# Optimization experiments

Hardware: AMD Instinct MI355X
Metric: run time of the kernel (lower is better)

## Reference

```python
import jax, jax.numpy as jnp
import numpy as np

B, N, M, D = 32, 1024, 576, 768

def setup_inputs() -> dict:
    key = jax.random.key(0)
    k1, k2 = jax.random.split(key)
    hidden_states = jax.random.normal(k1, (B, N, D), dtype=jnp.float32)
    img_hidden_state = jax.random.normal(k2, (B, M, D), dtype=jnp.float32)
    return {"hidden_states": hidden_states, "img_hidden_state": img_hidden_state}

def reference(hidden_states, img_hidden_state):
    # Unscaled cross-attention: softmax(Q K^T) V with Q=text, K=V=image features.
    scores = jnp.einsum('bnd,bmd->bnm', hidden_states, img_hidden_state)  # [B,N,M]
    probs = jax.nn.softmax(scores, axis=-1)
    fusion_output = jnp.einsum('bnm,bmd->bnd', probs, img_hidden_state)   # [B,N,D]
    return fusion_output
```

## Files before the change

### kernel.cpp

```cpp
#include <hip/hip_runtime.h>

typedef float f32x4 __attribute__((ext_vector_type(4)));
typedef _Float16 h8 __attribute__((ext_vector_type(8)));
typedef unsigned short us8 __attribute__((ext_vector_type(8)));

#define DEV __device__ __forceinline__
#define SBARRIER() asm volatile("s_barrier" ::: "memory")
#define LGKM0()    asm volatile("s_waitcnt lgkmcnt(0)" ::: "memory")
#define VMCNT3()   asm volatile("s_waitcnt vmcnt(3)" ::: "memory")
#define VMCNT0()   asm volatile("s_waitcnt vmcnt(0)" ::: "memory")
#define SCHED0()   __builtin_amdgcn_sched_barrier(0)

constexpr int Bb = 32, Nn = 1024, Mm = 576, Dd = 768;
constexpr float L2E = 1.44269504088896340736f;

constexpr size_t KF_ELEMS = (size_t)Bb * 36 * 24 * 512;

DEV unsigned short f2h(float x) {
  _Float16 h = (_Float16)x;
  return __builtin_bit_cast(unsigned short, h);
}
DEV void gll16(const void* g, void* l) {
  __builtin_amdgcn_global_load_lds(
      (const __attribute__((address_space(1))) void*)g,
      (__attribute__((address_space(3))) void*)l, 16, 0, 0);
}

__global__ __launch_bounds__(256)
void fusion_prep(const float* __restrict__ K, unsigned short* __restrict__ Kf,
                 unsigned short* __restrict__ Vf)
{
  __shared__ float ks[64][33];
  const int t   = threadIdx.x;
  const int blk = blockIdx.x;
  const int b    = blk / 18;
  const int r2   = blk % 18;
  const int rt   = r2 >> 1;
  const int half = r2 & 1;
  const int l    = t & 63;

  const int row0 = t >> 3, c40 = t & 7;
  const int row1 = (t + 256) >> 3;
  const float* Kb = K + ((size_t)(b * Mm + rt * 64)) * Dd;

  const int kvt_l = t >> 6;
  const int kf_r  = kvt_l * 16 + (l & 15);
  const int kf_c  = (l >> 4) * 8;
  const int kc_l = t >> 7;
  const int dtl  = (t >> 6) & 1;
  const int vf_r = kc_l * 32 + (l >> 4) * 8;
  const int vf_c = dtl * 16 + (l & 15);

#pragma unroll 1
  for (int dc = half * 12; dc < half * 12 + 12; ++dc) {
    __syncthreads();
    f32x4 v0 = *(const f32x4*)(Kb + (size_t)row0 * Dd + dc * 32 + c40 * 4);
    f32x4 v1 = *(const f32x4*)(Kb + (size_t)row1 * Dd + dc * 32 + c40 * 4);
    *(f32x4*)&ks[row0][c40 * 4] = v0;
    *(f32x4*)&ks[row1][c40 * 4] = v1;
    __syncthreads();
    {
      us8 h;
#pragma unroll
      for (int j = 0; j < 8; ++j) h[j] = f2h(ks[kf_r][kf_c + j]);
      *(us8*)&Kf[(((size_t)((b * 36 + rt * 4 + kvt_l) * 24 + dc)) << 9) + l * 8] = h;
    }
    {
      us8 o;
#pragma unroll
      for (int j = 0; j < 8; ++j) o[j] = f2h(ks[vf_r + j][vf_c]);
      *(us8*)&Vf[(((size_t)((b * 18 + rt * 2 + kc_l) * 48 + dc * 2 + dtl)) << 9) + l * 8] = o;
    }
  }
}

__global__ __launch_bounds__(1024, 1)
void fusion_main(const float* __restrict__ Q, const unsigned short* __restrict__ Kf,
                 const unsigned short* __restrict__ Vf, float* __restrict__ Out)
{
  __shared__ alignas(16) unsigned char lds[147456];
  __shared__ float sRa[4][128];
  __shared__ float sRb[4][128];

  const int tid  = threadIdx.x;
  const int lane = tid & 63;
  const int w    = tid >> 6;
  const int g    = lane >> 4;
  const int ln   = lane & 15;
  const int wq   = w >> 2;
  const int wkv  = w & 3;
  const int wq2  = w >> 3;
  const int wd8  = w & 7;

  const bool loader  = (w < 12);
  const bool qstager = (w >= 12);

  const int bid = blockIdx.x;
  const int xcd = bid & 7, ii = bid >> 3;
  const int b  = (xcd << 2) | (ii >> 3);
  const int q0 = (ii & 7) * 128;

  const float* Qb = Q + ((size_t)(b * Nn + q0)) * Dd;
  const unsigned char* KfB = (const unsigned char*)Kf + ((size_t)(b * 36 * 24) << 10);
  const unsigned short* VfB = Vf + ((size_t)(b * 18 * 48) << 9);

  const int u0 = w * 3;
  const int t256 = tid & 255;
  const int s0 = t256, s1 = t256 + 256;
  const int qt0 = s0 >> 6, l0 = s0 & 63;
  const int qt1 = s1 >> 6, l1 = s1 & 63;
  const float* qsrc0 = Qb + (size_t)(qt0 * 16 + (l0 & 15)) * Dd + (l0 >> 4) * 8;
  const float* qsrc1 = Qb + (size_t)(qt1 * 16 + (l1 & 15)) * Dd + (l1 >> 4) * 8;
  unsigned char* qd0 = lds + 110592 + qt0 * 1024 + l0 * 16;
  unsigned char* qd1 = lds + 110592 + qt1 * 1024 + l1 * 16;

  {
    f32x4 a0, a1, b0, b1;
    if (qstager) {
      a0 = *(const f32x4*)qsrc0; a1 = *(const f32x4*)(qsrc0 + 4);
      b0 = *(const f32x4*)qsrc1; b1 = *(const f32x4*)(qsrc1 + 4);
    }
    SCHED0();
    if (loader) {
#pragma unroll
      for (int j = 0; j < 3; ++j)
        gll16(KfB + ((size_t)((u0 + j) * 24) << 10) + (lane << 4), lds + (u0 + j) * 1024);
#pragma unroll
      for (int j = 0; j < 3; ++j)
        gll16(KfB + ((size_t)((u0 + j) * 24 + 1) << 10) + (lane << 4), lds + 36864 + (u0 + j) * 1024);
    }
    if (qstager) {
      us8 h0, h1;
#pragma unroll
      for (int k = 0; k < 4; ++k) {
        h0[k]   = f2h(a0[k] * L2E);
        h0[k+4] = f2h(a1[k] * L2E);
        h1[k]   = f2h(b0[k] * L2E);
        h1[k+4] = f2h(b1[k] * L2E);
      }
      *(us8*)qd0 = h0;
      *(us8*)qd1 = h1;
    }
    if (loader) { VMCNT3(); }
    LGKM0();
    SBARRIER();
    SCHED0();
  }

  f32x4 acc[2][9];
#pragma unroll
  for (int mt = 0; mt < 2; ++mt)
#pragma unroll
    for (int nt = 0; nt < 9; ++nt) acc[mt][nt] = (f32x4){0.f, 0.f, 0.f, 0.f};

#pragma unroll 1
  for (int c = 0; c < 24; ++c) {
    f32x4 a0, a1, b0, b1;
    if (qstager && c < 23) {
      const size_t off = (size_t)(c + 1) * 32;
      a0 = *(const f32x4*)(qsrc0 + off); a1 = *(const f32x4*)(qsrc0 + off + 4);
      b0 = *(const f32x4*)(qsrc1 + off); b1 = *(const f32x4*)(qsrc1 + off + 4);
    }
    SCHED0();
    if (loader && c < 22) {
      unsigned char* dst = lds + ((c + 2) % 3) * 36864;
#pragma unroll
      for (int j = 0; j < 3; ++j) {
        const int u = u0 + j;
        gll16(KfB + ((size_t)(u * 24 + c + 2) << 10) + (lane << 4), dst + u * 1024);
      }
    }
    const unsigned char* qb = lds + 110592 + (c & 1) * 8192;
    const unsigned char* kb = lds + (c % 3) * 36864;
    h8 qh[2];
#pragma unroll
    for (int mt = 0; mt < 2; ++mt)
      qh[mt] = *(const h8*)(qb + (wq * 2 + mt) * 1024 + lane * 16);
    __builtin_amdgcn_s_setprio(1);
#pragma unroll
    for (int nt = 0; nt < 9; ++nt) {
      const h8 kf = *(const h8*)(kb + (wkv * 9 + nt) * 1024 + lane * 16);
#pragma unroll
      for (int mt = 0; mt < 2; ++mt)
        acc[mt][nt] = __builtin_amdgcn_mfma_f32_16x16x32_f16(qh[mt], kf, acc[mt][nt], 0, 0, 0);
    }
    __builtin_amdgcn_s_setprio(0);
    SCHED0();
    if (qstager && c < 23) {
      us8 h0, h1;
#pragma unroll
      for (int k = 0; k < 4; ++k) {
        h0[k]   = f2h(a0[k] * L2E);
        h0[k+4] = f2h(a1[k] * L2E);
        h1[k]   = f2h(b0[k] * L2E);
        h1[k+4] = f2h(b1[k] * L2E);
      }
      *(us8*)(qd0 + ((c + 1) & 1) * 8192) = h0;
      *(us8*)(qd1 + ((c + 1) & 1) * 8192) = h1;
    }
    if (loader) {
      if (c <= 21) { VMCNT3(); }
      else         { VMCNT0(); }
    }
    LGKM0();
    SBARRIER();
    SCHED0();
  }

  float pm[2][4];
#pragma unroll
  for (int mt = 0; mt < 2; ++mt)
#pragma unroll
    for (int i2 = 0; i2 < 4; ++i2) {
      float v = acc[mt][0][i2];
#pragma unroll
      for (int nt = 1; nt < 9; ++nt) v = fmaxf(v, acc[mt][nt][i2]);
      pm[mt][i2] = v;
    }
#pragma unroll
  for (int mk = 1; mk < 16; mk <<= 1)
#pragma unroll
    for (int mt = 0; mt < 2; ++mt)
#pragma unroll
      for (int i2 = 0; i2 < 4; ++i2)
        pm[mt][i2] = fmaxf(pm[mt][i2], __shfl_xor(pm[mt][i2], mk, 64));
  if (ln == 0) {
#pragma unroll
    for (int mt = 0; mt < 2; ++mt)
#pragma unroll
      for (int i2 = 0; i2 < 4; ++i2)
        sRa[wkv][wq * 32 + mt * 16 + g * 4 + i2] = pm[mt][i2];
  }
  __syncthreads();

  float mfin[2][4], ps[2][4];
#pragma unroll
  for (int mt = 0; mt < 2; ++mt)
#pragma unroll
    for (int i2 = 0; i2 < 4; ++i2) {
      const int rw = wq * 32 + mt * 16 + g * 4 + i2;
      mfin[mt][i2] = fmaxf(fmaxf(sRa[0][rw], sRa[1][rw]), fmaxf(sRa[2][rw], sRa[3][rw]));
      ps[mt][i2] = 0.f;
    }
#pragma unroll
  for (int mt = 0; mt < 2; ++mt)
#pragma unroll
    for (int nt = 0; nt < 9; ++nt)
#pragma unroll
      for (int i2 = 0; i2 < 4; ++i2) {
        const float p = exp2f(acc[mt][nt][i2] - mfin[mt][i2]);
        acc[mt][nt][i2] = p;
        ps[mt][i2] += p;
      }
#pragma unroll
  for (int mk = 1; mk < 16; mk <<= 1)
#pragma unroll
    for (int mt = 0; mt < 2; ++mt)
#pragma unroll
      for (int i2 = 0; i2 < 4; ++i2)
        ps[mt][i2] += __shfl_xor(ps[mt][i2], mk, 64);
  if (ln == 0) {
#pragma unroll
    for (int mt = 0; mt < 2; ++mt)
#pragma unroll
      for (int i2 = 0; i2 < 4; ++i2)
        sRb[wkv][wq * 32 + mt * 16 + g * 4 + i2] = ps[mt][i2];
  }
  __syncthreads();

  {
    unsigned short* sPp = (unsigned short*)lds;
#pragma unroll
    for (int mt = 0; mt < 2; ++mt)
#pragma unroll
      for (int i2 = 0; i2 < 4; ++i2) {
        const int rw = wq * 32 + mt * 16 + g * 4 + i2;
        const float inv = 1.0f / ((sRb[0][rw] + sRb[1][rw]) + (sRb[2][rw] + sRb[3][rw]));
#pragma unroll
        for (int nt = 0; nt < 9; ++nt) {
          const int u = wkv * 18 + nt * 2 + (ln >> 3);
          sPp[rw * 576 + ((u ^ (rw & 7)) << 3) + (ln & 7)] = f2h(acc[mt][nt][i2] * inv);
        }
      }
  }
  __syncthreads();

#pragma unroll 1
  for (int p = 0; p < 2; ++p) {
    f32x4 O[4][3];
#pragma unroll
    for (int mt = 0; mt < 4; ++mt)
#pragma unroll
      for (int nt = 0; nt < 3; ++nt) O[mt][nt] = (f32x4){0.f, 0.f, 0.f, 0.f};

    const unsigned short* vbase = VfB + ((size_t)(wd8 * 6 + p * 3) << 9) + lane * 8;
    h8 vfA[3], vfB2[3];
#pragma unroll
    for (int nt = 0; nt < 3; ++nt)
      vfA[nt] = *(const h8*)(vbase + ((size_t)nt << 9));

#pragma unroll 1
    for (int kc = 0; kc < 18; kc += 2) {
#pragma unroll
      for (int nt = 0; nt < 3; ++nt)
        vfB2[nt] = *(const h8*)(vbase + ((size_t)((kc + 1) * 48 + nt) << 9));
      {
        h8 pa[4];
#pragma unroll
        for (int mt = 0; mt < 4; ++mt) {
          const int row = wq2 * 64 + mt * 16 + ln;
          const int u = kc * 4 + g;
          pa[mt] = *(const h8*)(lds + row * 1152 + ((u ^ (row & 7)) << 4));
        }
#pragma unroll
        for (int nt = 0; nt < 3; ++nt)
#pragma unroll
          for (int mt = 0; mt < 4; ++mt)
            O[mt][nt] = __builtin_amdgcn_mfma_f32_16x16x32_f16(pa[mt], vfA[nt], O[mt][nt], 0, 0, 0);
      }
      if (kc < 16) {
#pragma unroll
        for (int nt = 0; nt < 3; ++nt)
          vfA[nt] = *(const h8*)(vbase + ((size_t)((kc + 2) * 48 + nt) << 9));
      }
      {
        h8 pa[4];
#pragma unroll
        for (int mt = 0; mt < 4; ++mt) {
          const int row = wq2 * 64 + mt * 16 + ln;
          const int u = (kc + 1) * 4 + g;
          pa[mt] = *(const h8*)(lds + row * 1152 + ((u ^ (row & 7)) << 4));
        }
#pragma unroll
        for (int nt = 0; nt < 3; ++nt)
#pragma unroll
          for (int mt = 0; mt < 4; ++mt)
            O[mt][nt] = __builtin_amdgcn_mfma_f32_16x16x32_f16(pa[mt], vfB2[nt], O[mt][nt], 0, 0, 0);
      }
    }

    float* ob = Out + ((size_t)(b * Nn + q0 + wq2 * 64)) * Dd;
#pragma unroll
    for (int mt = 0; mt < 4; ++mt)
#pragma unroll
      for (int nt = 0; nt < 3; ++nt)
#pragma unroll
        for (int i2 = 0; i2 < 4; ++i2)
          ob[(size_t)(mt * 16 + g * 4 + i2) * Dd + wd8 * 96 + p * 48 + nt * 16 + ln] = O[mt][nt][i2];
  }
}

extern "C" void kernel_launch(void* const* d_in, const int* in_sizes, int n_in,
                              void* d_out, int out_size, void* d_ws, size_t ws_size,
                              hipStream_t stream) {
  const float* Q = (const float*)d_in[0];
  const float* K = (const float*)d_in[1];
  float* Out = (float*)d_out;
  unsigned short* Kf = (unsigned short*)d_ws;
  unsigned short* Vf = Kf + KF_ELEMS;
  fusion_prep<<<dim3(Bb * 18), dim3(256), 0, stream>>>(K, Kf, Vf);
  fusion_main<<<dim3(Bb * 8), dim3(1024), 0, stream>>>(Q, Kf, Vf, Out);
}
```

Measured before the change: 112.1 us.

## Halve block to 512 threads with larger per-wave tiles and double-buffered K

Shrinks the main kernel from 16 to 8 waves per block. Each wave now computes a 64-row score tile and a 64x96 output tile, and every wave both loads K and stages Q instead of splitting those roles across dedicated waves. The K pipeline goes from triple to double buffering and uses __syncthreads instead of hand-placed waitcnt and s_barrier. The intent is more register-level reuse of fragments and less LDS traffic per MFMA. The cost is half as many waves to hide latency and a shallower prefetch.

Result: slower. 118.6 us (+5.8%).

```diff
diff --git a/kernel.cpp b/kernel.cpp
--- a/kernel.cpp
+++ b/kernel.cpp
@@ -5,11 +5,6 @@
 typedef unsigned short us8 __attribute__((ext_vector_type(8)));
 
 #define DEV __device__ __forceinline__
-#define SBARRIER() asm volatile("s_barrier" ::: "memory")
-#define LGKM0()    asm volatile("s_waitcnt lgkmcnt(0)" ::: "memory")
-#define VMCNT3()   asm volatile("s_waitcnt vmcnt(3)" ::: "memory")
-#define VMCNT0()   asm volatile("s_waitcnt vmcnt(0)" ::: "memory")
-#define SCHED0()   __builtin_amdgcn_sched_barrier(0)
 
 constexpr int Bb = 32, Nn = 1024, Mm = 576, Dd = 768;
 constexpr float L2E = 1.44269504088896340736f;
@@ -74,7 +69,7 @@
   }
 }
 
-__global__ __launch_bounds__(1024, 1)
+__global__ __launch_bounds__(512, 1)
 void fusion_main(const float* __restrict__ Q, const unsigned short* __restrict__ Kf,
                  const unsigned short* __restrict__ Vf, float* __restrict__ Out)
 {
@@ -87,13 +82,10 @@
   const int w    = tid >> 6;
   const int g    = lane >> 4;
   const int ln   = lane & 15;
-  const int wq   = w >> 2;
+  const int wqk  = w >> 2;
   const int wkv  = w & 3;
-  const int wq2  = w >> 3;
-  const int wd8  = w & 7;
-
-  const bool loader  = (w < 12);
-  const bool qstager = (w >= 12);
+  const int wq2  = w >> 2;
+  const int wd4  = w & 3;
 
   const int bid = blockIdx.x;
   const int xcd = bid & 7, ii = bid >> 3;
@@ -104,112 +96,82 @@
   const unsigned char* KfB = (const unsigned char*)Kf + ((size_t)(b * 36 * 24) << 10);
   const unsigned short* VfB = Vf + ((size_t)(b * 18 * 48) << 9);
 
-  const int u0 = w * 3;
-  const int t256 = tid & 255;
-  const int s0 = t256, s1 = t256 + 256;
-  const int qt0 = s0 >> 6, l0 = s0 & 63;
-  const int qt1 = s1 >> 6, l1 = s1 & 63;
-  const float* qsrc0 = Qb + (size_t)(qt0 * 16 + (l0 & 15)) * Dd + (l0 >> 4) * 8;
-  const float* qsrc1 = Qb + (size_t)(qt1 * 16 + (l1 & 15)) * Dd + (l1 >> 4) * 8;
-  unsigned char* qd0 = lds + 110592 + qt0 * 1024 + l0 * 16;
-  unsigned char* qd1 = lds + 110592 + qt1 * 1024 + l1 * 16;
-
+  const int nu = (w < 4) ? 5 : 4;
+  const int u0 = (w < 4) ? w * 5 : 20 + (w - 4) * 4;
+
+  const int qt_s = tid >> 6;
+  const float* qsrc = Qb + (size_t)(qt_s * 16 + (lane & 15)) * Dd + (lane >> 4) * 8;
+  unsigned char* qdst = lds + 73728 + qt_s * 1024 + lane * 16;
+
+  f32x4 acc_init = (f32x4){0.f, 0.f, 0.f, 0.f};
   {
-    f32x4 a0, a1, b0, b1;
-    if (qstager) {
-      a0 = *(const f32x4*)qsrc0; a1 = *(const f32x4*)(qsrc0 + 4);
-      b0 = *(const f32x4*)qsrc1; b1 = *(const f32x4*)(qsrc1 + 4);
-    }
-    SCHED0();
-    if (loader) {
-#pragma unroll
-      for (int j = 0; j < 3; ++j)
+    f32x4 a0 = *(const f32x4*)qsrc;
+    f32x4 a1 = *(const f32x4*)(qsrc + 4);
+#pragma unroll
+    for (int j = 0; j < 5; ++j)
+      if (j < nu)
         gll16(KfB + ((size_t)((u0 + j) * 24) << 10) + (lane << 4), lds + (u0 + j) * 1024);
-#pragma unroll
-      for (int j = 0; j < 3; ++j)
-        gll16(KfB + ((size_t)((u0 + j) * 24 + 1) << 10) + (lane << 4), lds + 36864 + (u0 + j) * 1024);
-    }
-    if (qstager) {
-      us8 h0, h1;
+    us8 h0;
+#pragma unroll
+    for (int k = 0; k < 4; ++k) {
+      h0[k]   = f2h(a0[k] * L2E);
+      h0[k+4] = f2h(a1[k] * L2E);
+    }
+    *(us8*)qdst = h0;
+    __syncthreads();
+  }
+
+  f32x4 acc[4][9];
+#pragma unroll
+  for (int mt = 0; mt < 4; ++mt)
+#pragma unroll
+    for (int nt = 0; nt < 9; ++nt) acc[mt][nt] = acc_init;
+
+#pragma unroll 1
+  for (int c = 0; c < 24; ++c) {
+    const int cur = c & 1, nxt = cur ^ 1;
+    const bool stg = (c < 23);
+    f32x4 a0, a1;
+    if (stg) {
+      const float* qs = qsrc + (size_t)(c + 1) * 32;
+      a0 = *(const f32x4*)qs;
+      a1 = *(const f32x4*)(qs + 4);
+#pragma unroll
+      for (int j = 0; j < 5; ++j)
+        if (j < nu)
+          gll16(KfB + ((size_t)((u0 + j) * 24 + c + 1) << 10) + (lane << 4),
+                lds + nxt * 36864 + (u0 + j) * 1024);
+    }
+    const unsigned char* qb = lds + 73728 + cur * 8192;
+    const unsigned char* kb = lds + cur * 36864;
+    h8 qh[4];
+#pragma unroll
+    for (int mt = 0; mt < 4; ++mt)
+      qh[mt] = *(const h8*)(qb + (wqk * 4 + mt) * 1024 + lane * 16);
+    __builtin_amdgcn_s_setprio(1);
+#pragma unroll
+    for (int nt = 0; nt < 9; ++nt) {
+      const h8 kf = *(const h8*)(kb + (wkv * 9 + nt) * 1024 + lane * 16);
+#pragma unroll
+      for (int mt = 0; mt < 4; ++mt)
+        acc[mt][nt] = __builtin_amdgcn_mfma_f32_16x16x32_f16(qh[mt], kf, acc[mt][nt], 0, 0, 0);
+    }
+    __builtin_amdgcn_s_setprio(0);
+    if (stg) {
+      us8 h0;
 #pragma unroll
       for (int k = 0; k < 4; ++k) {
         h0[k]   = f2h(a0[k] * L2E);
         h0[k+4] = f2h(a1[k] * L2E);
-        h1[k]   = f2h(b0[k] * L2E);
-        h1[k+4] = f2h(b1[k] * L2E);
-      }
-      *(us8*)qd0 = h0;
-      *(us8*)qd1 = h1;
-    }
-    if (loader) { VMCNT3(); }
-    LGKM0();
-    SBARRIER();
-    SCHED0();
-  }
-
-  f32x4 acc[2][9];
-#pragma unroll
-  for (int mt = 0; mt < 2; ++mt)
-#pragma unroll
-    for (int nt = 0; nt < 9; ++nt) acc[mt][nt] = (f32x4){0.f, 0.f, 0.f, 0.f};
-
-#pragma unroll 1
-  for (int c = 0; c < 24; ++c) {
-    f32x4 a0, a1, b0, b1;
-    if (qstager && c < 23) {
-      const size_t off = (size_t)(c + 1) * 32;
-      a0 = *(const f32x4*)(qsrc0 + off); a1 = *(const f32x4*)(qsrc0 + off + 4);
-      b0 = *(const f32x4*)(qsrc1 + off); b1 = *(const f32x4*)(qsrc1 + off + 4);
-    }
-    SCHED0();
-    if (loader && c < 22) {
-      unsigned char* dst = lds + ((c + 2) % 3) * 36864;
-#pragma unroll
-      for (int j = 0; j < 3; ++j) {
-        const int u = u0 + j;
-        gll16(KfB + ((size_t)(u * 24 + c + 2) << 10) + (lane << 4), dst + u * 1024);
-      }
-    }
-    const unsigned char* qb = lds + 110592 + (c & 1) * 8192;
-    const unsigned char* kb = lds + (c % 3) * 36864;
-    h8 qh[2];
-#pragma unroll
-    for (int mt = 0; mt < 2; ++mt)
-      qh[mt] = *(const h8*)(qb + (wq * 2 + mt) * 1024 + lane * 16);
-    __builtin_amdgcn_s_setprio(1);
-#pragma unroll
-    for (int nt = 0; nt < 9; ++nt) {
-      const h8 kf = *(const h8*)(kb + (wkv * 9 + nt) * 1024 + lane * 16);
-#pragma unroll
-      for (int mt = 0; mt < 2; ++mt)
-        acc[mt][nt] = __builtin_amdgcn_mfma_f32_16x16x32_f16(qh[mt], kf, acc[mt][nt], 0, 0, 0);
-    }
-    __builtin_amdgcn_s_setprio(0);
-    SCHED0();
-    if (qstager && c < 23) {
-      us8 h0, h1;
-#pragma unroll
-      for (int k = 0; k < 4; ++k) {
-        h0[k]   = f2h(a0[k] * L2E);
-        h0[k+4] = f2h(a1[k] * L2E);
-        h1[k]   = f2h(b0[k] * L2E);
-        h1[k+4] = f2h(b1[k] * L2E);
-      }
-      *(us8*)(qd0 + ((c + 1) & 1) * 8192) = h0;
-      *(us8*)(qd1 + ((c + 1) & 1) * 8192) = h1;
-    }
-    if (loader) {
-      if (c <= 21) { VMCNT3(); }
-      else         { VMCNT0(); }
-    }
-    LGKM0();
-    SBARRIER();
-    SCHED0();
-  }
-
-  float pm[2][4];
-#pragma unroll
-  for (int mt = 0; mt < 2; ++mt)
+      }
+      *(us8*)(qdst + nxt * 8192) = h0;
+    }
+    __syncthreads();
+  }
+
+  float pm[4][4];
+#pragma unroll
+  for (int mt = 0; mt < 4; ++mt)
 #pragma unroll
     for (int i2 = 0; i2 < 4; ++i2) {
       float v = acc[mt][0][i2];
@@ -220,30 +182,30 @@
 #pragma unroll
   for (int mk = 1; mk < 16; mk <<= 1)
 #pragma unroll
-    for (int mt = 0; mt < 2; ++mt)
+    for (int mt = 0; mt < 4; ++mt)
 #pragma unroll
       for (int i2 = 0; i2 < 4; ++i2)
         pm[mt][i2] = fmaxf(pm[mt][i2], __shfl_xor(pm[mt][i2], mk, 64));
   if (ln == 0) {
 #pragma unroll
-    for (int mt = 0; mt < 2; ++mt)
+    for (int mt = 0; mt < 4; ++mt)
 #pragma unroll
       for (int i2 = 0; i2 < 4; ++i2)
-        sRa[wkv][wq * 32 + mt * 16 + g * 4 + i2] = pm[mt][i2];
+        sRa[wkv][wqk * 64 + mt * 16 + g * 4 + i2] = pm[mt][i2];
   }
   __syncthreads();
 
-  float mfin[2][4], ps[2][4];
-#pragma unroll
-  for (int mt = 0; mt < 2; ++mt)
+  float mfin[4][4], ps[4][4];
+#pragma unroll
+  for (int mt = 0; mt < 4; ++mt)
 #pragma unroll
     for (int i2 = 0; i2 < 4; ++i2) {
-      const int rw = wq * 32 + mt * 16 + g * 4 + i2;
+      const int rw = wqk * 64 + mt * 16 + g * 4 + i2;
       mfin[mt][i2] = fmaxf(fmaxf(sRa[0][rw], sRa[1][rw]), fmaxf(sRa[2][rw], sRa[3][rw]));
       ps[mt][i2] = 0.f;
     }
 #pragma unroll
-  for (int mt = 0; mt < 2; ++mt)
+  for (int mt = 0; mt < 4; ++mt)
 #pragma unroll
     for (int nt = 0; nt < 9; ++nt)
 #pragma unroll
@@ -255,26 +217,26 @@
 #pragma unroll
   for (int mk = 1; mk < 16; mk <<= 1)
 #pragma unroll
-    for (int mt = 0; mt < 2; ++mt)
+    for (int mt = 0; mt < 4; ++mt)
 #pragma unroll
       for (int i2 = 0; i2 < 4; ++i2)
         ps[mt][i2] += __shfl_xor(ps[mt][i2], mk, 64);
   if (ln == 0) {
 #pragma unroll
-    for (int mt = 0; mt < 2; ++mt)
+    for (int mt = 0; mt < 4; ++mt)
 #pragma unroll
       for (int i2 = 0; i2 < 4; ++i2)
-        sRb[wkv][wq * 32 + mt * 16 + g * 4 + i2] = ps[mt][i2];
+        sRb[wkv][wqk * 64 + mt * 16 + g * 4 + i2] = ps[mt][i2];
   }
   __syncthreads();
 
   {
     unsigned short* sPp = (unsigned short*)lds;
 #pragma unroll
-    for (int mt = 0; mt < 2; ++mt)
+    for (int mt = 0; mt < 4; ++mt)
 #pragma unroll
       for (int i2 = 0; i2 < 4; ++i2) {
-        const int rw = wq * 32 + mt * 16 + g * 4 + i2;
+        const int rw = wqk * 64 + mt * 16 + g * 4 + i2;
         const float inv = 1.0f / ((sRb[0][rw] + sRb[1][rw]) + (sRb[2][rw] + sRb[3][rw]));
 #pragma unroll
         for (int nt = 0; nt < 9; ++nt) {
@@ -287,22 +249,22 @@
 
 #pragma unroll 1
   for (int p = 0; p < 2; ++p) {
-    f32x4 O[4][3];
-#pragma unroll
-    for (int mt = 0; mt < 4; ++mt)
-#pragma unroll
-      for (int nt = 0; nt < 3; ++nt) O[mt][nt] = (f32x4){0.f, 0.f, 0.f, 0.f};
-
-    const unsigned short* vbase = VfB + ((size_t)(wd8 * 6 + p * 3) << 9) + lane * 8;
-    h8 vfA[3], vfB2[3];
-#pragma unroll
-    for (int nt = 0; nt < 3; ++nt)
+    f32x4 O[4][6];
+#pragma unroll
+    for (int mt = 0; mt < 4; ++mt)
+#pragma unroll
+      for (int nt = 0; nt < 6; ++nt) O[mt][nt] = (f32x4){0.f, 0.f, 0.f, 0.f};
+
+    const unsigned short* vbase = VfB + ((size_t)(wd4 * 12 + p * 6) << 9) + lane * 8;
+    h8 vfA[6], vfB2[6];
+#pragma unroll
+    for (int nt = 0; nt < 6; ++nt)
       vfA[nt] = *(const h8*)(vbase + ((size_t)nt << 9));
 
 #pragma unroll 1
     for (int kc = 0; kc < 18; kc += 2) {
 #pragma unroll
-      for (int nt = 0; nt < 3; ++nt)
+      for (int nt = 0; nt < 6; ++nt)
         vfB2[nt] = *(const h8*)(vbase + ((size_t)((kc + 1) * 48 + nt) << 9));
       {
         h8 pa[4];
@@ -313,14 +275,14 @@
           pa[mt] = *(const h8*)(lds + row * 1152 + ((u ^ (row & 7)) << 4));
         }
 #pragma unroll
-        for (int nt = 0; nt < 3; ++nt)
+        for (int nt = 0; nt < 6; ++nt)
 #pragma unroll
           for (int mt = 0; mt < 4; ++mt)
             O[mt][nt] = __builtin_amdgcn_mfma_f32_16x16x32_f16(pa[mt], vfA[nt], O[mt][nt], 0, 0, 0);
       }
       if (kc < 16) {
 #pragma unroll
-        for (int nt = 0; nt < 3; ++nt)
+        for (int nt = 0; nt < 6; ++nt)
           vfA[nt] = *(const h8*)(vbase + ((size_t)((kc + 2) * 48 + nt) << 9));
       }
       {
@@ -332,7 +294,7 @@
           pa[mt] = *(const h8*)(lds + row * 1152 + ((u ^ (row & 7)) << 4));
         }
 #pragma unroll
-        for (int nt = 0; nt < 3; ++nt)
+        for (int nt = 0; nt < 6; ++nt)
 #pragma unroll
           for (int mt = 0; mt < 4; ++mt)
             O[mt][nt] = __builtin_amdgcn_mfma_f32_16x16x32_f16(pa[mt], vfB2[nt], O[mt][nt], 0, 0, 0);
@@ -343,10 +305,10 @@
 #pragma unroll
     for (int mt = 0; mt < 4; ++mt)
 #pragma unroll
-      for (int nt = 0; nt < 3; ++nt)
+      for (int nt = 0; nt < 6; ++nt)
 #pragma unroll
         for (int i2 = 0; i2 < 4; ++i2)
-          ob[(size_t)(mt * 16 + g * 4 + i2) * Dd + wd8 * 96 + p * 48 + nt * 16 + ln] = O[mt][nt][i2];
+          ob[(size_t)(mt * 16 + g * 4 + i2) * Dd + wd4 * 192 + p * 96 + nt * 16 + ln] = O[mt][nt][i2];
   }
 }
 
@@ -359,5 +321,5 @@
   unsigned short* Kf = (unsigned short*)d_ws;
   unsigned short* Vf = Kf + KF_ELEMS;
   fusion_prep<<<dim3(Bb * 18), dim3(256), 0, stream>>>(K, Kf, Vf);
-  fusion_main<<<dim3(Bb * 8), dim3(1024), 0, stream>>>(Q, Kf, Vf, Out);
-}
+  fusion_main<<<dim3(Bb * 8), dim3(512), 0, stream>>>(Q, Kf, Vf, Out);
+}
```

## Split QK chunk loop into three phases interleaving LDS reads, global loads and MFMAs

Applied to the files above, without the earlier changes.

Restructures the per-chunk QK^T loop into three phases of three N-tiles each. Each phase first prefetches its K fragments into registers and issues one global-to-LDS load, then runs its MFMAs, with barriers between phases. The aim is to overlap memory traffic with matrix math, in the style of a ping-pong schedule across waves. It adds extra s_barriers per chunk, which could cost more in synchronisation than the overlap saves.

Result: slower. 130.4 us (+16.3%).

```diff
diff --git a/kernel.cpp b/kernel.cpp
--- a/kernel.cpp
+++ b/kernel.cpp
@@ -155,37 +155,61 @@
 
 #pragma unroll 1
   for (int c = 0; c < 24; ++c) {
+    const unsigned char* qb = lds + 110592 + (c & 1) * 8192;
+    const unsigned char* kb = lds + (c % 3) * 36864;
+    unsigned char* dstK = lds + ((c + 2) % 3) * 36864;
+    const bool stgK = loader && (c < 22);
     f32x4 a0, a1, b0, b1;
+
+    h8 qh[2];
+#pragma unroll
+    for (int mt = 0; mt < 2; ++mt)
+      qh[mt] = *(const h8*)(qb + (wq * 2 + mt) * 1024 + lane * 16);
+    h8 kfr[3];
+#pragma unroll
+    for (int nt = 0; nt < 3; ++nt)
+      kfr[nt] = *(const h8*)(kb + (wkv * 9 + nt) * 1024 + lane * 16);
     if (qstager && c < 23) {
       const size_t off = (size_t)(c + 1) * 32;
       a0 = *(const f32x4*)(qsrc0 + off); a1 = *(const f32x4*)(qsrc0 + off + 4);
       b0 = *(const f32x4*)(qsrc1 + off); b1 = *(const f32x4*)(qsrc1 + off + 4);
     }
-    SCHED0();
-    if (loader && c < 22) {
-      unsigned char* dst = lds + ((c + 2) % 3) * 36864;
-#pragma unroll
-      for (int j = 0; j < 3; ++j) {
-        const int u = u0 + j;
-        gll16(KfB + ((size_t)(u * 24 + c + 2) << 10) + (lane << 4), dst + u * 1024);
-      }
-    }
-    const unsigned char* qb = lds + 110592 + (c & 1) * 8192;
-    const unsigned char* kb = lds + (c % 3) * 36864;
-    h8 qh[2];
-#pragma unroll
-    for (int mt = 0; mt < 2; ++mt)
-      qh[mt] = *(const h8*)(qb + (wq * 2 + mt) * 1024 + lane * 16);
+    if (stgK)
+      gll16(KfB + ((size_t)(u0 * 24 + c + 2) << 10) + (lane << 4), dstK + u0 * 1024);
+    SBARRIER();
+    LGKM0();
+    SCHED0();
     __builtin_amdgcn_s_setprio(1);
 #pragma unroll
-    for (int nt = 0; nt < 9; ++nt) {
-      const h8 kf = *(const h8*)(kb + (wkv * 9 + nt) * 1024 + lane * 16);
+    for (int nt = 0; nt < 3; ++nt)
 #pragma unroll
       for (int mt = 0; mt < 2; ++mt)
-        acc[mt][nt] = __builtin_amdgcn_mfma_f32_16x16x32_f16(qh[mt], kf, acc[mt][nt], 0, 0, 0);
-    }
+        acc[mt][nt] = __builtin_amdgcn_mfma_f32_16x16x32_f16(qh[mt], kfr[nt], acc[mt][nt], 0, 0, 0);
     __builtin_amdgcn_s_setprio(0);
-    SCHED0();
+    SBARRIER();
+
+#pragma unroll
+    for (int nt = 0; nt < 3; ++nt)
+      kfr[nt] = *(const h8*)(kb + (wkv * 9 + 3 + nt) * 1024 + lane * 16);
+    if (stgK)
+      gll16(KfB + ((size_t)((u0 + 1) * 24 + c + 2) << 10) + (lane << 4), dstK + (u0 + 1) * 1024);
+    SBARRIER();
+    LGKM0();
+    SCHED0();
+    __builtin_amdgcn_s_setprio(1);
+#pragma unroll
+    for (int nt = 0; nt < 3; ++nt)
+#pragma unroll
+      for (int mt = 0; mt < 2; ++mt)
+        acc[mt][3 + nt] = __builtin_amdgcn_mfma_f32_16x16x32_f16(qh[mt], kfr[nt], acc[mt][3 + nt], 0, 0, 0);
+    __builtin_amdgcn_s_setprio(0);
+    SBARRIER();
+
+#pragma unroll
+    for (int nt = 0; nt < 3; ++nt)
+      kfr[nt] = *(const h8*)(kb + (wkv * 9 + 6 + nt) * 1024 + lane * 16);
+    if (stgK)
+      gll16(KfB + ((size_t)((u0 + 2) * 24 + c + 2) << 10) + (lane << 4), dstK + (u0 + 2) * 1024);
     if (qstager && c < 23) {
       us8 h0, h1;
 #pragma unroll
@@ -198,6 +222,17 @@
       *(us8*)(qd0 + ((c + 1) & 1) * 8192) = h0;
       *(us8*)(qd1 + ((c + 1) & 1) * 8192) = h1;
     }
+    SBARRIER();
+    LGKM0();
+    SCHED0();
+    __builtin_amdgcn_s_setprio(1);
+#pragma unroll
+    for (int nt = 0; nt < 3; ++nt)
+#pragma unroll
+      for (int mt = 0; mt < 2; ++mt)
+        acc[mt][6 + nt] = __builtin_amdgcn_mfma_f32_16x16x32_f16(qh[mt], kfr[nt], acc[mt][6 + nt], 0, 0, 0);
+    __builtin_amdgcn_s_setprio(0);
+
     if (loader) {
       if (c <= 21) { VMCNT3(); }
       else         { VMCNT0(); }
```
